# Kernel optimization log

Hardware: AMD Instinct MI355X
Metric: run time of the kernel (lower is better)

The kernel has to match this reference:

```python
import jax, jax.numpy as jnp
import numpy as np

DIM = 2048
DIM_HEAD = 64
HEADS = 16
FF_MULT = 4
LORA_R = 8
ATTN_INNER = DIM_HEAD * HEADS            # 1024
FF_INNER = DIM * FF_MULT                 # 8192
FUSED_DIMS = (ATTN_INNER, DIM_HEAD, DIM_HEAD, FF_INNER * 2)
B, N = 2, 2048


def setup_inputs() -> dict:
    key = jax.random.key(0)
    ks = jax.random.split(key, 12)
    s = 0.02
    inp = {
        "x": jax.random.normal(ks[0], (B, N, DIM), dtype=jnp.float32),
        "gamma": jnp.ones((DIM,), dtype=jnp.float32),
        "w_fused": jax.random.normal(ks[1], (DIM, sum(FUSED_DIMS)), dtype=jnp.float32) * s,
        "w_attn_out": jax.random.normal(ks[2], (ATTN_INNER, DIM), dtype=jnp.float32) * s,
        "w_ff_out": jax.random.normal(ks[3], (FF_INNER, DIM), dtype=jnp.float32) * s,
        "lora_q_a": jax.random.normal(ks[4], (DIM, LORA_R), dtype=jnp.float32) * s,
        "lora_q_b": jax.random.normal(ks[5], (LORA_R, ATTN_INNER), dtype=jnp.float32) * s,
        "lora_k_a": jax.random.normal(ks[6], (DIM, LORA_R), dtype=jnp.float32) * s,
        "lora_k_b": jax.random.normal(ks[7], (LORA_R, DIM_HEAD), dtype=jnp.float32) * s,
        "lora_v_a": jax.random.normal(ks[8], (DIM, LORA_R), dtype=jnp.float32) * s,
        "lora_v_b": jax.random.normal(ks[9], (LORA_R, DIM_HEAD), dtype=jnp.float32) * s,
        "lora_o_a": jax.random.normal(ks[10], (ATTN_INNER, LORA_R), dtype=jnp.float32) * s,
        "lora_o_b": jax.random.normal(ks[11], (LORA_R, DIM), dtype=jnp.float32) * s,
    }
    return inp


def _rotate_half(x):
    x1, x2 = jnp.split(x, 2, axis=-1)
    return jnp.concatenate((-x2, x1), axis=-1)


def _rope(pos, t):
    return t * jnp.cos(pos) + _rotate_half(t) * jnp.sin(pos)


def _forward(x, gamma, w_fused, w_attn_out, w_ff_out,
             lora_q_a, lora_q_b, lora_k_a, lora_k_b,
             lora_v_a, lora_v_b, lora_o_a, lora_o_b):
    b, n, d = x.shape
    # LayerNorm (beta = 0)
    mu = jnp.mean(x, axis=-1, keepdims=True)
    var = jnp.var(x, axis=-1, keepdims=True)
    xn = (x - mu) * jax.lax.rsqrt(var + 1e-5) * gamma

    fused = xn @ w_fused
    i0, i1, i2 = np.cumsum(FUSED_DIMS)[:3]
    q, k, v, ff = fused[..., :i0], fused[..., i0:i1], fused[..., i1:i2], fused[..., i2:]

    # LoRA additive terms
    q = q + (xn @ lora_q_a) @ lora_q_b
    k = k + (xn @ lora_k_a) @ lora_k_b
    v = v + (xn @ lora_v_a) @ lora_v_b

    q = q.reshape(b, n, HEADS, DIM_HEAD).transpose(0, 2, 1, 3)  # b h n d
    q = q * (DIM_HEAD ** -0.5)

    # rotary embedding: pos (n, dim_head)
    inv_freq = 1.0 / (10000.0 ** (jnp.arange(0, DIM_HEAD, 2, dtype=jnp.float32) / DIM_HEAD))
    freqs = jnp.arange(n, dtype=jnp.float32)[:, None] * inv_freq[None, :]
    pos = jnp.concatenate((freqs, freqs), axis=-1)
    q = _rope(pos, q)
    k = _rope(pos, k)  # k is b n d (multi-query, single kv head)

    sim = jnp.einsum('bhid,bjd->bhij', q, k)
    causal = jnp.triu(jnp.ones((n, n), dtype=bool), k=1)
    sim = jnp.where(causal, -jnp.finfo(sim.dtype).max, sim)
    attn = jax.nn.softmax(sim, axis=-1)
    out = jnp.einsum('bhij,bjd->bhid', attn, v)
    out = out.transpose(0, 2, 1, 3).reshape(b, n, ATTN_INNER)

    attn_out = out @ w_attn_out + (out @ lora_o_a) @ lora_o_b

    # SwiGLU: chunk -> (x_ff, gate); silu(gate) * x_ff
    x_ff, gate = jnp.split(ff, 2, axis=-1)
    ff_out = (jax.nn.silu(gate) * x_ff) @ w_ff_out

    return attn_out + ff_out


def reference(x, gamma, w_fused, w_attn_out, w_ff_out,
              lora_q_a, lora_q_b, lora_k_a, lora_k_b,
              lora_v_a, lora_v_b, lora_o_a, lora_o_b):
    return _forward(x, gamma, w_fused, w_attn_out, w_ff_out,
                    lora_q_a, lora_q_b, lora_k_a, lora_k_b,
                    lora_v_a, lora_v_b, lora_o_a, lora_o_b)
```

## Files before the change

kernel.cpp:

```cpp
#include <hip/hip_runtime.h>
#include <cstdint>


typedef __bf16 bf16_t;
typedef __bf16 bf16x8 __attribute__((ext_vector_type(8)));
typedef float f32x4 __attribute__((ext_vector_type(4)));

#define LOG2E 1.44269504088896340736f
#define LOG2_10K 13.287712379549449f

__device__ __forceinline__ void gload_lds16(const void* g, void* l) {
  __builtin_amdgcn_global_load_lds(
      (__attribute__((address_space(1))) void*)(uintptr_t)g,
      (__attribute__((address_space(3))) void*)(uint32_t)(uintptr_t)l,
      16, 0, 0);
}

__device__ __forceinline__ f32x4 mfma16(bf16x8 a, bf16x8 b, f32x4 c) {
  return __builtin_amdgcn_mfma_f32_16x16x32_bf16(a, b, c, 0, 0, 0);
}

__global__ __launch_bounds__(256) void ln_kernel(
    const float* __restrict__ x, const float* __restrict__ gamma,
    bf16_t* __restrict__ xn)
{
  const int row = blockIdx.x;
  const int t = threadIdx.x;
  const float4* xr = (const float4*)(x + (size_t)row * 2048);
  float4 a = xr[t * 2];
  float4 b = xr[t * 2 + 1];
  float s  = a.x + a.y + a.z + a.w + b.x + b.y + b.z + b.w;
  float ss = a.x*a.x + a.y*a.y + a.z*a.z + a.w*a.w
           + b.x*b.x + b.y*b.y + b.z*b.z + b.w*b.w;
  #pragma unroll
  for (int m = 1; m < 64; m <<= 1) {
    s  += __shfl_xor(s, m);
    ss += __shfl_xor(ss, m);
  }
  __shared__ float red[8];
  const int wave = t >> 6, lane = t & 63;
  if (lane == 0) { red[wave] = s; red[4 + wave] = ss; }
  __syncthreads();
  const float stot  = red[0] + red[1] + red[2] + red[3];
  const float sstot = red[4] + red[5] + red[6] + red[7];
  const float mu  = stot * (1.f / 2048.f);
  const float var = sstot * (1.f / 2048.f) - mu * mu;
  const float rs  = rsqrtf(var + 1e-5f);
  float v[8] = {a.x, a.y, a.z, a.w, b.x, b.y, b.z, b.w};
  bf16x8 o;
  #pragma unroll
  for (int e = 0; e < 8; ++e)
    o[e] = (bf16_t)((v[e] - mu) * rs * gamma[t * 8 + e]);
  *(bf16x8*)(xn + (size_t)row * 2048 + t * 8) = o;
}

__global__ __launch_bounds__(256) void transpose_wf_kernel(
    const float* __restrict__ w,
    const float* __restrict__ qa, const float* __restrict__ qb,
    const float* __restrict__ ka, const float* __restrict__ kb,
    const float* __restrict__ va, const float* __restrict__ vb,
    bf16_t* __restrict__ wfT)
{
  __shared__ float tile[64][65];
  const int t  = threadIdx.x;
  const int n0 = blockIdx.x * 64;
  const int k0 = blockIdx.y * 64;
  #pragma unroll
  for (int it = 0; it < 4; ++it) {
    const int kr = (t >> 4) + it * 16;
    const float4 vv = *(const float4*)(w + (size_t)(k0 + kr) * 17536 + n0 + (t & 15) * 4);
    tile[kr][(t & 15) * 4 + 0] = vv.x;
    tile[kr][(t & 15) * 4 + 1] = vv.y;
    tile[kr][(t & 15) * 4 + 2] = vv.z;
    tile[kr][(t & 15) * 4 + 3] = vv.w;
  }
  __syncthreads();
  const float* la = nullptr; const float* lb = nullptr;
  int nbo = 0, ldlb = 0;
  if (n0 < 1024)      { la = qa; lb = qb; nbo = n0;        ldlb = 1024; }
  else if (n0 < 1088) { la = ka; lb = kb; nbo = n0 - 1024; ldlb = 64;   }
  else if (n0 < 1152) { la = va; lb = vb; nbo = n0 - 1088; ldlb = 64;   }
  #pragma unroll
  for (int it = 0; it < 2; ++it) {
    const int nl = (t >> 3) + it * 32;
    const int kl = (t & 7) * 8;
    float vals[8];
    #pragma unroll
    for (int e = 0; e < 8; ++e) vals[e] = tile[kl + e][nl];
    if (la) {
      float bc[8];
      #pragma unroll
      for (int r = 0; r < 8; ++r) bc[r] = lb[r * ldlb + nbo + nl];
      #pragma unroll
      for (int e = 0; e < 8; ++e) {
        const float* ar = la + (size_t)(k0 + kl + e) * 8;
        float d = 0.f;
        #pragma unroll
        for (int r = 0; r < 8; ++r) d += ar[r] * bc[r];
        vals[e] += d;
      }
    }
    bf16x8 o;
    #pragma unroll
    for (int e = 0; e < 8; ++e) o[e] = (bf16_t)vals[e];
    *(bf16x8*)(wfT + (size_t)(n0 + nl) * 2048 + k0 + kl) = o;
  }
}

__global__ __launch_bounds__(256) void transpose_w2_kernel(
    const float* __restrict__ wff,
    const float* __restrict__ watt,
    const float* __restrict__ oa, const float* __restrict__ ob,
    bf16_t* __restrict__ w2T)
{
  __shared__ float tile[64][65];
  const int t  = threadIdx.x;
  const int n0 = blockIdx.x * 64;
  const int k0 = blockIdx.y * 64;
  const bool isatt = (k0 >= 8192);
  const float* src = isatt ? (watt + (size_t)(k0 - 8192) * 2048)
                           : (wff + (size_t)k0 * 2048);
  #pragma unroll
  for (int it = 0; it < 4; ++it) {
    const int kr = (t >> 4) + it * 16;
    const float4 vv = *(const float4*)(src + (size_t)kr * 2048 + n0 + (t & 15) * 4);
    tile[kr][(t & 15) * 4 + 0] = vv.x;
    tile[kr][(t & 15) * 4 + 1] = vv.y;
    tile[kr][(t & 15) * 4 + 2] = vv.z;
    tile[kr][(t & 15) * 4 + 3] = vv.w;
  }
  __syncthreads();
  #pragma unroll
  for (int it = 0; it < 2; ++it) {
    const int nl = (t >> 3) + it * 32;
    const int kl = (t & 7) * 8;
    float vals[8];
    #pragma unroll
    for (int e = 0; e < 8; ++e) vals[e] = tile[kl + e][nl];
    if (isatt) {
      float bc[8];
      #pragma unroll
      for (int r = 0; r < 8; ++r) bc[r] = ob[r * 2048 + n0 + nl];
      #pragma unroll
      for (int e = 0; e < 8; ++e) {
        const float* ar = oa + (size_t)(k0 - 8192 + kl + e) * 8;
        float d = 0.f;
        #pragma unroll
        for (int r = 0; r < 8; ++r) d += ar[r] * bc[r];
        vals[e] += d;
      }
    }
    bf16x8 o;
    #pragma unroll
    for (int e = 0; e < 8; ++e) o[e] = (bf16_t)vals[e];
    *(bf16x8*)(w2T + (size_t)(n0 + nl) * 9216 + k0 + kl) = o;
  }
}

__device__ __forceinline__ void gemm_core_128x128(
    const bf16_t* __restrict__ A, int ldA, int m0,
    const bf16_t* __restrict__ BT, int ldB, int n0,
    int K, bf16_t* As, bf16_t* Bs, f32x4* acc)
{
  const int t = threadIdx.x;
  const int wave = t >> 6;
  const int lane = t & 63;
  const int quad = lane >> 4;
  const int ln15 = lane & 15;
  const int wm = wave & 1, wn = wave >> 1;

  const bf16_t* gA = A + (size_t)(m0 + (t >> 2)) * ldA + ((t & 3) << 3);
  const bf16_t* gB = BT + (size_t)(n0 + (t >> 2)) * ldB + ((t & 3) << 3);
  char* lA = (char*)As + wave * 1024;
  char* lB = (char*)Bs + wave * 1024;
  const size_t sA64 = (size_t)64 * ldA;
  const size_t sB64 = (size_t)64 * ldB;
  const int aoff = (wm * 64 + ln15) * 32 + quad * 8;
  const int boff = (wn * 64 + ln15) * 32 + quad * 8;

  for (int kt = 0; kt < K; kt += 32) {
    gload_lds16(gA,        lA);
    gload_lds16(gA + sA64, lA + 4096);
    gload_lds16(gB,        lB);
    gload_lds16(gB + sB64, lB + 4096);
    gA += 32;
    gB += 32;
    __syncthreads();
    bf16x8 a0 = *(const bf16x8*)(As + aoff);
    bf16x8 a1 = *(const bf16x8*)(As + aoff + 512);
    bf16x8 a2 = *(const bf16x8*)(As + aoff + 1024);
    bf16x8 a3 = *(const bf16x8*)(As + aoff + 1536);
    bf16x8 b0 = *(const bf16x8*)(Bs + boff);
    bf16x8 b1 = *(const bf16x8*)(Bs + boff + 512);
    bf16x8 b2 = *(const bf16x8*)(Bs + boff + 1024);
    bf16x8 b3 = *(const bf16x8*)(Bs + boff + 1536);
    acc[0]  = mfma16(a0, b0, acc[0]);
    acc[1]  = mfma16(a0, b1, acc[1]);
    acc[2]  = mfma16(a0, b2, acc[2]);
    acc[3]  = mfma16(a0, b3, acc[3]);
    acc[4]  = mfma16(a1, b0, acc[4]);
    acc[5]  = mfma16(a1, b1, acc[5]);
    acc[6]  = mfma16(a1, b2, acc[6]);
    acc[7]  = mfma16(a1, b3, acc[7]);
    acc[8]  = mfma16(a2, b0, acc[8]);
    acc[9]  = mfma16(a2, b1, acc[9]);
    acc[10] = mfma16(a2, b2, acc[10]);
    acc[11] = mfma16(a2, b3, acc[11]);
    acc[12] = mfma16(a3, b0, acc[12]);
    acc[13] = mfma16(a3, b1, acc[13]);
    acc[14] = mfma16(a3, b2, acc[14]);
    acc[15] = mfma16(a3, b3, acc[15]);
    __syncthreads();
  }
}

__device__ __forceinline__ void gemm_core_dual(
    const bf16_t* gA, const bf16_t* gB0, const bf16_t* gB1,
    int ldA, int ldB, int K,
    bf16_t* As, bf16_t* B0s, bf16_t* B1s,
    f32x4* acc0, f32x4* acc1)
{
  const int t = threadIdx.x;
  const int wave = t >> 6;
  const int lane = t & 63;
  const int quad = lane >> 4;
  const int ln15 = lane & 15;
  const int wm = wave & 1, wn = wave >> 1;

  char* lA = (char*)As + wave * 1024;
  char* l0 = (char*)B0s + wave * 1024;
  char* l1 = (char*)B1s + wave * 1024;
  const size_t sA64 = (size_t)64 * ldA;
  const size_t sB64 = (size_t)64 * ldB;
  const int aoff = (wm * 64 + ln15) * 32 + quad * 8;
  const int boff = (wn * 64 + ln15) * 32 + quad * 8;

  for (int kt = 0; kt < K; kt += 32) {
    gload_lds16(gA,         lA);
    gload_lds16(gA + sA64,  lA + 4096);
    gload_lds16(gB0,        l0);
    gload_lds16(gB0 + sB64, l0 + 4096);
    gload_lds16(gB1,        l1);
    gload_lds16(gB1 + sB64, l1 + 4096);
    gA += 32; gB0 += 32; gB1 += 32;
    __syncthreads();
    bf16x8 a0 = *(const bf16x8*)(As + aoff);
    bf16x8 a1 = *(const bf16x8*)(As + aoff + 512);
    bf16x8 a2 = *(const bf16x8*)(As + aoff + 1024);
    bf16x8 a3 = *(const bf16x8*)(As + aoff + 1536);
    bf16x8 p0 = *(const bf16x8*)(B0s + boff);
    bf16x8 p1 = *(const bf16x8*)(B0s + boff + 512);
    bf16x8 p2 = *(const bf16x8*)(B0s + boff + 1024);
    bf16x8 p3 = *(const bf16x8*)(B0s + boff + 1536);
    bf16x8 q0 = *(const bf16x8*)(B1s + boff);
    bf16x8 q1 = *(const bf16x8*)(B1s + boff + 512);
    bf16x8 q2 = *(const bf16x8*)(B1s + boff + 1024);
    bf16x8 q3 = *(const bf16x8*)(B1s + boff + 1536);
    acc0[0]  = mfma16(a0, p0, acc0[0]);
    acc0[1]  = mfma16(a0, p1, acc0[1]);
    acc0[2]  = mfma16(a0, p2, acc0[2]);
    acc0[3]  = mfma16(a0, p3, acc0[3]);
    acc1[0]  = mfma16(a0, q0, acc1[0]);
    acc1[1]  = mfma16(a0, q1, acc1[1]);
    acc1[2]  = mfma16(a0, q2, acc1[2]);
    acc1[3]  = mfma16(a0, q3, acc1[3]);
    acc0[4]  = mfma16(a1, p0, acc0[4]);
    acc0[5]  = mfma16(a1, p1, acc0[5]);
    acc0[6]  = mfma16(a1, p2, acc0[6]);
    acc0[7]  = mfma16(a1, p3, acc0[7]);
    acc1[4]  = mfma16(a1, q0, acc1[4]);
    acc1[5]  = mfma16(a1, q1, acc1[5]);
    acc1[6]  = mfma16(a1, q2, acc1[6]);
    acc1[7]  = mfma16(a1, q3, acc1[7]);
    acc0[8]  = mfma16(a2, p0, acc0[8]);
    acc0[9]  = mfma16(a2, p1, acc0[9]);
    acc0[10] = mfma16(a2, p2, acc0[10]);
    acc0[11] = mfma16(a2, p3, acc0[11]);
    acc1[8]  = mfma16(a2, q0, acc1[8]);
    acc1[9]  = mfma16(a2, q1, acc1[9]);
    acc1[10] = mfma16(a2, q2, acc1[10]);
    acc1[11] = mfma16(a2, q3, acc1[11]);
    acc0[12] = mfma16(a3, p0, acc0[12]);
    acc0[13] = mfma16(a3, p1, acc0[13]);
    acc0[14] = mfma16(a3, p2, acc0[14]);
    acc0[15] = mfma16(a3, p3, acc0[15]);
    acc1[12] = mfma16(a3, q0, acc1[12]);
    acc1[13] = mfma16(a3, q1, acc1[13]);
    acc1[14] = mfma16(a3, q2, acc1[14]);
    acc1[15] = mfma16(a3, q3, acc1[15]);
    __syncthreads();
  }
}

__global__ __launch_bounds__(256, 2) void gemm1_qkv_kernel(
    const bf16_t* __restrict__ xn, const bf16_t* __restrict__ wfT,
    bf16_t* __restrict__ Q, bf16_t* __restrict__ K, bf16_t* __restrict__ Vt)
{
  __shared__ __align__(16) bf16_t As[128 * 32];
  __shared__ __align__(16) bf16_t B0s[128 * 32];
  __shared__ __align__(16) bf16_t B1s[128 * 32];
  const int m0 = blockIdx.x * 128;
  const int y = blockIdx.y;
  const int t = threadIdx.x;
  const int wave = t >> 6, lane = t & 63;
  const int quad = lane >> 4, ln15 = lane & 15;
  const int wm = wave & 1, wn = wave >> 1;

  const int rb = m0 + wm * 64 + quad * 4;
  const float invf0 = exp2f(-(float)ln15 * (LOG2_10K / 32.0f));
  const float invf1 = exp2f(-(float)(16 + ln15) * (LOG2_10K / 32.0f));

  if (y < 4) {
    const bf16_t* gA  = xn  + (size_t)(m0 + (t >> 2)) * 2048 + ((t & 3) << 3);
    const bf16_t* gB0 = wfT + (size_t)(y * 256 + (t >> 2)) * 2048 + ((t & 3) << 3);
    const bf16_t* gB1 = wfT + (size_t)(y * 256 + 128 + (t >> 2)) * 2048 + ((t & 3) << 3);
    f32x4 acc0[16], acc1[16];
    #pragma unroll
    for (int f = 0; f < 16; ++f) {
      acc0[f] = (f32x4){0.f, 0.f, 0.f, 0.f};
      acc1[f] = (f32x4){0.f, 0.f, 0.f, 0.f};
    }
    gemm_core_dual(gA, gB0, gB1, 2048, 2048, 2048, As, B0s, B1s, acc0, acc1);
    #pragma unroll
    for (int half = 0; half < 2; ++half) {
      const f32x4* acc = half ? acc1 : acc0;
      const int hd = y * 4 + half * 2 + wn;
      #pragma unroll
      for (int i = 0; i < 4; ++i) {
        #pragma unroll
        for (int rr = 0; rr < 4; ++rr) {
          const int row = rb + i * 16 + rr;
          const int b = row >> 11, n = row & 2047;
          const float fn = (float)n;
          float s0, c0, s1, c1;
          __sincosf(fn * invf0, &s0, &c0);
          __sincosf(fn * invf1, &s1, &c1);
          float vals[4];
          #pragma unroll
          for (int j = 0; j < 4; ++j) vals[j] = acc[i * 4 + j][rr];
          #pragma unroll
          for (int j = 0; j < 4; ++j) {
            const float rot = (j < 2) ? -vals[j + 2] : vals[j - 2];
            const float c = (j & 1) ? c1 : c0;
            const float s = (j & 1) ? s1 : s0;
            const float o = (vals[j] * c + rot * s) * 0.125f;
            Q[(((size_t)b * 16 + hd) * 2048 + n) * 64 + j * 16 + ln15] = (bf16_t)o;
          }
        }
      }
    }
  } else {
    f32x4 acc[16];
    #pragma unroll
    for (int f = 0; f < 16; ++f) acc[f] = (f32x4){0.f, 0.f, 0.f, 0.f};
    gemm_core_128x128(xn, 2048, m0, wfT, 2048, 1024, 2048, As, B0s, acc);
    const bool is_k = (wn == 0);
    #pragma unroll
    for (int i = 0; i < 4; ++i) {
      #pragma unroll
      for (int rr = 0; rr < 4; ++rr) {
        const int row = rb + i * 16 + rr;
        const int b = row >> 11, n = row & 2047;
        float vals[4];
        #pragma unroll
        for (int j = 0; j < 4; ++j) vals[j] = acc[i * 4 + j][rr];
        if (is_k) {
          const float fn = (float)n;
          float s0, c0, s1, c1;
          __sincosf(fn * invf0, &s0, &c0);
          __sincosf(fn * invf1, &s1, &c1);
          #pragma unroll
          for (int j = 0; j < 4; ++j) {
            const float rot = (j < 2) ? -vals[j + 2] : vals[j - 2];
            const float c = (j & 1) ? c1 : c0;
            const float s = (j & 1) ? s1 : s0;
            K[((size_t)b * 2048 + n) * 64 + j * 16 + ln15] = (bf16_t)(vals[j] * c + rot * s);
          }
        } else {
          #pragma unroll
          for (int j = 0; j < 4; ++j)
            Vt[((size_t)b * 64 + j * 16 + ln15) * 2048 + n] = (bf16_t)vals[j];
        }
      }
    }
  }
}


#define FF_STG() {                                                           \
    char* lA_ = lds + sst + w * 1024;                                        \
    gload_lds16(gA, lA_);                                                    \
    gload_lds16(gA + (size_t)128 * 2048, lA_ + 8192);                        \
    char* lB_ = lds + 65536 + sst + w * 1024;                                \
    gload_lds16(gB0, lB_);                                                   \
    gload_lds16(gB1, lB_ + 8192);                                            \
    gA += 32; gB0 += 32; gB1 += 32;                                          \
    sst = (sst + 16384) & 65535; }

#define FF_RD(DA, DB) {                                                      \
    _Pragma("unroll")                                                        \
    for (int mf_ = 0; mf_ < 8; ++mf_)                                        \
      DA[mf_] = *(const bf16x8*)(lds + srd + wm * 8192 + mf_ * 1024 + ro);   \
    _Pragma("unroll")                                                        \
    for (int nf_ = 0; nf_ < 4; ++nf_)                                        \
      DB[nf_] = *(const bf16x8*)(lds + 65536 + srd + wn * 4096 + nf_ * 1024 + ro); \
    srd = (srd + 16384) & 65535; }

#define FF_MM(SA, SB) {                                                      \
    __builtin_amdgcn_s_setprio(1);                                           \
    _Pragma("unroll")                                                        \
    for (int mf_ = 0; mf_ < 8; ++mf_) {                                      \
      _Pragma("unroll")                                                      \
      for (int nf_ = 0; nf_ < 4; ++nf_)                                      \
        acc[mf_][nf_] = mfma16(SA[mf_], SB[nf_], acc[mf_][nf_]);             \
    }                                                                        \
    __builtin_amdgcn_s_setprio(0); }

#define FF_SYNC4() { asm volatile("s_waitcnt vmcnt(4)" ::: "memory");        \
    __builtin_amdgcn_s_barrier(); }

__global__ __launch_bounds__(512, 2) void gemm1_ff_kernel(
    const bf16_t* __restrict__ xn, const bf16_t* __restrict__ wfT,
    bf16_t* __restrict__ A2)
{
  __shared__ __align__(16) char lds[131072];
  const int m0 = blockIdx.x * 256;
  const int c0 = blockIdx.y * 128;
  const int t = threadIdx.x;
  const int w = t >> 6, lane = t & 63;
  const int quad = lane >> 4, ln15 = lane & 15;
  const int wm = w & 1, wn = w >> 1;

  const int p  = w * 64 + lane;
  const int r  = p >> 2;
  const int cl = (p & 3) ^ ((r >> 1) & 3);
  const bf16_t* gA = xn + (size_t)(m0 + r) * 2048 + cl * 8;
  const int r2 = r + 128;
  const int cm0 = c0 + ((r  >> 5) << 4) + (r  & 15);
  const int cm1 = c0 + ((r2 >> 5) << 4) + (r2 & 15);
  const int wr0 = ((r  >> 4) & 1) ? (1152 + cm0) : (9344 + cm0);
  const int wr1 = ((r2 >> 4) & 1) ? (1152 + cm1) : (9344 + cm1);
  const bf16_t* gB0 = wfT + (size_t)wr0 * 2048 + cl * 8;
  const bf16_t* gB1 = wfT + (size_t)wr1 * 2048 + cl * 8;

  const int ro = ln15 * 64 + ((quad ^ ((ln15 >> 1) & 3)) * 16);

  f32x4 acc[8][4];
  #pragma unroll
  for (int mf = 0; mf < 8; ++mf)
    #pragma unroll
    for (int nf = 0; nf < 4; ++nf)
      acc[mf][nf] = (f32x4){0.f, 0.f, 0.f, 0.f};

  int sst = 0, srd = 0;
  #pragma unroll
  for (int pt = 0; pt < 3; ++pt) FF_STG();
  FF_SYNC4();

  bf16x8 fA[8], fB[4], nA[8], nB[4];
  FF_RD(fA, fB);

  for (int i = 0; i < 30; ++i) {
    FF_STG(); FF_RD(nA, nB); FF_MM(fA, fB); FF_SYNC4();
    FF_STG(); FF_RD(fA, fB); FF_MM(nA, nB); FF_SYNC4();
  }
  FF_STG(); FF_RD(nA, nB); FF_MM(fA, fB); FF_SYNC4();
  FF_RD(fA, fB); FF_MM(nA, nB);
  asm volatile("s_waitcnt vmcnt(0)" ::: "memory");
  __builtin_amdgcn_s_barrier();
  FF_RD(nA, nB); FF_MM(fA, fB);
  FF_MM(nA, nB);

  const int row0 = m0 + wm * 128 + quad * 4;
  const int col0 = c0 + wn * 32 + ln15;
  #pragma unroll
  for (int mf = 0; mf < 8; ++mf)
    #pragma unroll
    for (int rr = 0; rr < 4; ++rr) {
      bf16_t* dst = A2 + (size_t)(row0 + mf * 16 + rr) * 9216 + col0;
      #pragma unroll
      for (int j = 0; j < 2; ++j) {
        const float g  = acc[mf][2 * j][rr];
        const float xv = acc[mf][2 * j + 1][rr];
        dst[j * 16] = (bf16_t)(xv * (g / (1.f + exp2f(-g * LOG2E))));
      }
    }
}

#define G2_STG() {                                                           \
    char* lA_ = lds + sstA + w * 1024;                                       \
    gload_lds16(gA, lA_);                                                    \
    gload_lds16(gA + (size_t)128 * 9216, lA_ + 8192);                        \
    gload_lds16(gB, lds + 65536 + sstB + w * 1024);                          \
    gA += 32; gB += 32;                                                      \
    sstA = (sstA + 16384) & 65535;                                           \
    sstB = (sstB + 8192) & 32767; }

#define G2_RD(DA, DB) {                                                      \
    _Pragma("unroll")                                                        \
    for (int mf_ = 0; mf_ < 4; ++mf_)                                        \
      DA[mf_] = *(const bf16x8*)(lds + srdA + wm * 4096 + mf_ * 1024 + ro);  \
    _Pragma("unroll")                                                        \
    for (int nf_ = 0; nf_ < 4; ++nf_)                                        \
      DB[nf_] = *(const bf16x8*)(lds + 65536 + srdB + wn * 4096 + nf_ * 1024 + ro); \
    srdA = (srdA + 16384) & 65535;                                           \
    srdB = (srdB + 8192) & 32767; }

#define G2_MM(SA, SB) {                                                      \
    __builtin_amdgcn_s_setprio(1);                                           \
    _Pragma("unroll")                                                        \
    for (int mf_ = 0; mf_ < 4; ++mf_) {                                      \
      _Pragma("unroll")                                                      \
      for (int nf_ = 0; nf_ < 4; ++nf_)                                      \
        acc[mf_][nf_] = mfma16(SA[mf_], SB[nf_], acc[mf_][nf_]);             \
    }                                                                        \
    __builtin_amdgcn_s_setprio(0); }

#define G2_SYNC3() { asm volatile("s_waitcnt vmcnt(3)" ::: "memory");        \
    __builtin_amdgcn_s_barrier(); }

__global__ __launch_bounds__(512, 2) void gemm2_kernel(
    const bf16_t* __restrict__ A2, const bf16_t* __restrict__ w2T,
    float* __restrict__ out)
{
  __shared__ __align__(16) char lds[98304];
  const int m0 = blockIdx.x * 256;
  const int n0 = blockIdx.y * 128;
  const int t = threadIdx.x;
  const int w = t >> 6, lane = t & 63;
  const int quad = lane >> 4, ln15 = lane & 15;
  const int wm = w & 3, wn = w >> 2;

  const int p  = w * 64 + lane;
  const int r  = p >> 2;
  const int cl = (p & 3) ^ ((r >> 1) & 3);
  const bf16_t* gA = A2  + (size_t)(m0 + r) * 9216 + cl * 8;
  const bf16_t* gB = w2T + (size_t)(n0 + r) * 9216 + cl * 8;

  const int ro = ln15 * 64 + ((quad ^ ((ln15 >> 1) & 3)) * 16);

  f32x4 acc[4][4];
  #pragma unroll
  for (int mf = 0; mf < 4; ++mf)
    #pragma unroll
    for (int nf = 0; nf < 4; ++nf)
      acc[mf][nf] = (f32x4){0.f, 0.f, 0.f, 0.f};

  int sstA = 0, sstB = 0, srdA = 0, srdB = 0;
  #pragma unroll
  for (int pt = 0; pt < 3; ++pt) G2_STG();
  G2_SYNC3();

  bf16x8 fA[4], fB[4], nA[4], nB[4];
  G2_RD(fA, fB);

  for (int i = 0; i < 142; ++i) {
    G2_STG(); G2_RD(nA, nB); G2_MM(fA, fB); G2_SYNC3();
    G2_STG(); G2_RD(fA, fB); G2_MM(nA, nB); G2_SYNC3();
  }
  G2_STG(); G2_RD(nA, nB); G2_MM(fA, fB); G2_SYNC3();
  G2_RD(fA, fB); G2_MM(nA, nB);
  asm volatile("s_waitcnt vmcnt(0)" ::: "memory");
  __builtin_amdgcn_s_barrier();
  G2_RD(nA, nB); G2_MM(fA, fB);
  G2_MM(nA, nB);

  const int row0 = m0 + wm * 64 + quad * 4;
  const int col0 = n0 + wn * 64 + ln15;
  #pragma unroll
  for (int mf = 0; mf < 4; ++mf)
    #pragma unroll
    for (int rr = 0; rr < 4; ++rr) {
      float* dst = out + (size_t)(row0 + mf * 16 + rr) * 2048 + col0;
      #pragma unroll
      for (int nf = 0; nf < 4; ++nf)
        dst[nf * 16] = acc[mf][nf][rr];
    }
}

__global__ __launch_bounds__(256, 2) void attn_kernel(
    const bf16_t* __restrict__ Q, const bf16_t* __restrict__ Kg_,
    const bf16_t* __restrict__ Vt, bf16_t* __restrict__ A2)
{
  __shared__ __align__(16) bf16_t Qs[64 * 64];
  __shared__ __align__(16) bf16_t Ks[64 * 64];
  __shared__ __align__(16) bf16_t Vs[64 * 64];
  __shared__ __align__(16) bf16_t Ps[64 * 64];
  const int pidx = blockIdx.x, bh = blockIdx.y;
  const int b = bh >> 4, h = bh & 15;
  const int t = threadIdx.x;
  const int wave = t >> 6, lane = t & 63;
  const int quad = lane >> 4, ln15 = lane & 15;

  const bf16_t* Kg = Kg_ + (size_t)b * 2048 * 64;
  const bf16_t* Vg = Vt + (size_t)b * 64 * 2048;

  for (int hlf = 0; hlf < 2; ++hlf) {
    const int qt = hlf ? (31 - pidx) : pidx;
    const int qm0 = qt * 64;
    const bf16_t* Qg = Q + ((size_t)bh * 2048 + qm0) * 64;

    {
      const bf16_t* g = Qg + (size_t)(t >> 3) * 64 + ((t & 7) << 3);
      char* l = (char*)Qs + wave * 1024;
      gload_lds16(g,           l);
      gload_lds16(g + 32 * 64, l + 4096);
    }

    float mstate[4], lstate[4];
    f32x4 o_acc[4];
    #pragma unroll
    for (int rr = 0; rr < 4; ++rr) { mstate[rr] = -1e30f; lstate[rr] = 0.f; }
    #pragma unroll
    for (int jd = 0; jd < 4; ++jd) o_acc[jd] = (f32x4){0.f, 0.f, 0.f, 0.f};

    const int njt = qt + 1;
    for (int jt = 0; jt < njt; ++jt) {
      {
        const bf16_t* kg = Kg + (size_t)(jt * 64 + (t >> 3)) * 64 + ((t & 7) << 3);
        char* lk = (char*)Ks + wave * 1024;
        gload_lds16(kg,           lk);
        gload_lds16(kg + 32 * 64, lk + 4096);
        const bf16_t* vg = Vg + (size_t)(t >> 3) * 2048 + jt * 64 + ((t & 7) << 3);
        char* lv = (char*)Vs + wave * 1024;
        gload_lds16(vg,                   lv);
        gload_lds16(vg + (size_t)32*2048, lv + 4096);
      }
      __syncthreads();

      f32x4 sA[4];
      #pragma unroll
      for (int j = 0; j < 4; ++j) sA[j] = (f32x4){0.f, 0.f, 0.f, 0.f};
      #pragma unroll
      for (int ks = 0; ks < 2; ++ks) {
        bf16x8 aq = *(const bf16x8*)(Qs + (wave * 16 + ln15) * 64 + ks * 32 + quad * 8);
        #pragma unroll
        for (int j = 0; j < 4; ++j) {
          bf16x8 bk = *(const bf16x8*)(Ks + (j * 16 + ln15) * 64 + ks * 32 + quad * 8);
          sA[j] = mfma16(aq, bk, sA[j]);
        }
      }

      const bool needmask = (jt * 64 + 63 > qm0 + wave * 16);
      const int row0 = qm0 + wave * 16 + quad * 4;
      float alpha[4];
      #pragma unroll
      for (int rr = 0; rr < 4; ++rr) {
        const int rowg = row0 + rr;
        if (needmask) {
          #pragma unroll
          for (int j = 0; j < 4; ++j) {
            const int colg = jt * 64 + j * 16 + ln15;
            if (colg > rowg) sA[j][rr] = -1e30f;
          }
        }
        float mx = fmaxf(fmaxf(sA[0][rr], sA[1][rr]),
                         fmaxf(sA[2][rr], sA[3][rr]));
        mx = fmaxf(mx, __shfl_xor(mx, 1));
        mx = fmaxf(mx, __shfl_xor(mx, 2));
        mx = fmaxf(mx, __shfl_xor(mx, 4));
        mx = fmaxf(mx, __shfl_xor(mx, 8));
        const float mold = mstate[rr];
        const float mnew = fmaxf(mold, mx);
        const float al = exp2f((mold - mnew) * LOG2E);
        float rsum = 0.f;
        #pragma unroll
        for (int j = 0; j < 4; ++j) {
          const float p = exp2f((sA[j][rr] - mnew) * LOG2E);
          sA[j][rr] = p;
          rsum += p;
        }
        rsum += __shfl_xor(rsum, 1);
        rsum += __shfl_xor(rsum, 2);
        rsum += __shfl_xor(rsum, 4);
        rsum += __shfl_xor(rsum, 8);
        lstate[rr] = lstate[rr] * al + rsum;
        mstate[rr] = mnew;
        alpha[rr] = al;
      }
      #pragma unroll
      for (int jd = 0; jd < 4; ++jd)
        #pragma unroll
        for (int rr = 0; rr < 4; ++rr)
          o_acc[jd][rr] *= alpha[rr];
      #pragma unroll
      for (int j = 0; j < 4; ++j)
        #pragma unroll
        for (int rr = 0; rr < 4; ++rr)
          Ps[wave * 1024 + (quad * 4 + rr) * 64 + j * 16 + ln15] = (bf16_t)sA[j][rr];

      #pragma unroll
      for (int ks = 0; ks < 2; ++ks) {
        bf16x8 ap = *(const bf16x8*)(Ps + wave * 1024 + ln15 * 64 + ks * 32 + quad * 8);
        #pragma unroll
        for (int jd = 0; jd < 4; ++jd) {
          bf16x8 bv = *(const bf16x8*)(Vs + (jd * 16 + ln15) * 64 + ks * 32 + quad * 8);
          o_acc[jd] = mfma16(ap, bv, o_acc[jd]);
        }
      }
      __syncthreads();
    }

    const int row0 = qm0 + wave * 16 + quad * 4;
    #pragma unroll
    for (int rr = 0; rr < 4; ++rr) {
      const float inv = 1.f / lstate[rr];
      bf16_t* dst = A2 + ((size_t)b * 2048 + row0 + rr) * 9216 + 8192 + h * 64 + ln15;
      #pragma unroll
      for (int jd = 0; jd < 4; ++jd)
        dst[jd * 16] = (bf16_t)(o_acc[jd][rr] * inv);
    }
  }
}

extern "C" void kernel_launch(void* const* d_in, const int* in_sizes, int n_in,
                              void* d_out, int out_size, void* d_ws, size_t ws_size,
                              hipStream_t stream)
{
  const float* x      = (const float*)d_in[0];
  const float* gamma  = (const float*)d_in[1];
  const float* wfused = (const float*)d_in[2];
  const float* watt   = (const float*)d_in[3];
  const float* wff    = (const float*)d_in[4];
  const float* qa     = (const float*)d_in[5];
  const float* qb     = (const float*)d_in[6];
  const float* ka     = (const float*)d_in[7];
  const float* kb     = (const float*)d_in[8];
  const float* va     = (const float*)d_in[9];
  const float* vb     = (const float*)d_in[10];
  const float* oa     = (const float*)d_in[11];
  const float* ob     = (const float*)d_in[12];
  float* out = (float*)d_out;

  char* ws = (char*)d_ws;
  bf16_t* xn  = (bf16_t*)(ws);
  bf16_t* wfT = (bf16_t*)(ws + 16777216);
  bf16_t* w2T = (bf16_t*)(ws + 88604672);
  bf16_t* A2  = (bf16_t*)(ws + 126353408);
  bf16_t* Qr  = (bf16_t*)(ws + 201850880);
  bf16_t* Kr  = (bf16_t*)(ws + 210239488);
  bf16_t* Vtr = (bf16_t*)(ws + 210763776);

  ln_kernel<<<dim3(4096), dim3(256), 0, stream>>>(x, gamma, xn);
  transpose_wf_kernel<<<dim3(274, 32), dim3(256), 0, stream>>>(
      wfused, qa, qb, ka, kb, va, vb, wfT);
  transpose_w2_kernel<<<dim3(32, 144), dim3(256), 0, stream>>>(
      wff, watt, oa, ob, w2T);
  gemm1_qkv_kernel<<<dim3(32, 5), dim3(256), 0, stream>>>(xn, wfT, Qr, Kr, Vtr);
  gemm1_ff_kernel<<<dim3(16, 64), dim3(512), 0, stream>>>(xn, wfT, A2);
  attn_kernel<<<dim3(16, 32), dim3(256), 0, stream>>>(Qr, Kr, Vtr, A2);
  gemm2_kernel<<<dim3(16, 16), dim3(512), 0, stream>>>(A2, w2T, out);
}
```

Baseline: 876.9 us.

## Restructure GEMM pipelines into triple-buffered split phases and smaller gemm2 tiles

The FF GEMM main loop is reorganized into two half-phases per K-step: one stages A and computes the first half of the M fragments, the other stages B and computes the second half. Barriers sit between the LDS reads and the MFMAs, and a sched_barrier fences them, so fragment registers drop to one set and LDS drops to three buffers. gemm2 moves to 128x128 tiles with 256 threads and 4 blocks per CU, using the same triple-buffered single-phase pipeline. The aim is better overlap of global-to-LDS loads with MFMA and higher occupancy, at the cost of more barriers per K-step and more A/B reloads for the smaller gemm2 tiles.

After: 897.1 us. +2.3%, slower.

```diff
diff --git a/kernel.cpp b/kernel.cpp
--- a/kernel.cpp
+++ b/kernel.cpp
@@ -8,6 +8,9 @@
 
 #define LOG2E 1.44269504088896340736f
 #define LOG2_10K 13.287712379549449f
+
+#define WAITCNT_VM(N) __builtin_amdgcn_s_waitcnt(0x0F70 | (N))
+#define WAITCNT_LGKM() __builtin_amdgcn_s_waitcnt(0xC07F)
 
 __device__ __forceinline__ void gload_lds16(const void* g, void* l) {
   __builtin_amdgcn_global_load_lds(
@@ -387,43 +390,59 @@
 }
 
 
-#define FF_STG() {                                                           \
-    char* lA_ = lds + sst + w * 1024;                                        \
-    gload_lds16(gA, lA_);                                                    \
-    gload_lds16(gA + (size_t)128 * 2048, lA_ + 8192);                        \
-    char* lB_ = lds + 65536 + sst + w * 1024;                                \
-    gload_lds16(gB0, lB_);                                                   \
-    gload_lds16(gB1, lB_ + 8192);                                            \
-    gA += 32; gB0 += 32; gB1 += 32;                                          \
-    sst = (sst + 16384) & 65535; }
-
-#define FF_RD(DA, DB) {                                                      \
-    _Pragma("unroll")                                                        \
-    for (int mf_ = 0; mf_ < 8; ++mf_)                                        \
-      DA[mf_] = *(const bf16x8*)(lds + srd + wm * 8192 + mf_ * 1024 + ro);   \
+#define FF_PHA(STG) {                                                        \
+    if (STG) {                                                               \
+      char* d_ = lds + nb + w * 1024;                                        \
+      gload_lds16(gA, d_);                                                   \
+      gload_lds16(gA + (size_t)128 * 2048, d_ + 8192);                       \
+    }                                                                        \
     _Pragma("unroll")                                                        \
     for (int nf_ = 0; nf_ < 4; ++nf_)                                        \
-      DB[nf_] = *(const bf16x8*)(lds + 65536 + srd + wn * 4096 + nf_ * 1024 + ro); \
-    srd = (srd + 16384) & 65535; }
-
-#define FF_MM(SA, SB) {                                                      \
+      fB[nf_] = *(const bf16x8*)(lds + cb + 16384 + wn * 4096 + nf_ * 1024 + ro); \
+    _Pragma("unroll")                                                        \
+    for (int mf_ = 0; mf_ < 4; ++mf_)                                        \
+      fA[mf_] = *(const bf16x8*)(lds + cb + wm * 8192 + mf_ * 1024 + ro);    \
+    __builtin_amdgcn_s_barrier();                                            \
+    WAITCNT_LGKM();                                                          \
+    __builtin_amdgcn_sched_barrier(0);                                       \
     __builtin_amdgcn_s_setprio(1);                                           \
     _Pragma("unroll")                                                        \
-    for (int mf_ = 0; mf_ < 8; ++mf_) {                                      \
+    for (int mf_ = 0; mf_ < 4; ++mf_) {                                      \
       _Pragma("unroll")                                                      \
       for (int nf_ = 0; nf_ < 4; ++nf_)                                      \
-        acc[mf_][nf_] = mfma16(SA[mf_], SB[nf_], acc[mf_][nf_]);             \
+        acc[mf_][nf_] = mfma16(fA[mf_], fB[nf_], acc[mf_][nf_]);             \
     }                                                                        \
-    __builtin_amdgcn_s_setprio(0); }
-
-#define FF_SYNC4() { asm volatile("s_waitcnt vmcnt(4)" ::: "memory");        \
+    __builtin_amdgcn_s_setprio(0);                                           \
+    __builtin_amdgcn_s_barrier(); }
+
+#define FF_PHB(STG, VMW) {                                                   \
+    if (STG) {                                                               \
+      char* d_ = lds + nb + 16384 + w * 1024;                                \
+      gload_lds16(gB0, d_);                                                  \
+      gload_lds16(gB1, d_ + 8192);                                           \
+    }                                                                        \
+    _Pragma("unroll")                                                        \
+    for (int mf_ = 0; mf_ < 4; ++mf_)                                        \
+      fA[mf_] = *(const bf16x8*)(lds + cb + wm * 8192 + (4 + mf_) * 1024 + ro); \
+    __builtin_amdgcn_s_barrier();                                            \
+    WAITCNT_LGKM();                                                          \
+    __builtin_amdgcn_sched_barrier(0);                                       \
+    __builtin_amdgcn_s_setprio(1);                                           \
+    _Pragma("unroll")                                                        \
+    for (int mf_ = 0; mf_ < 4; ++mf_) {                                      \
+      _Pragma("unroll")                                                      \
+      for (int nf_ = 0; nf_ < 4; ++nf_)                                      \
+        acc[4 + mf_][nf_] = mfma16(fA[mf_], fB[nf_], acc[4 + mf_][nf_]);     \
+    }                                                                        \
+    __builtin_amdgcn_s_setprio(0);                                           \
+    VMW;                                                                     \
     __builtin_amdgcn_s_barrier(); }
 
 __global__ __launch_bounds__(512, 2) void gemm1_ff_kernel(
     const bf16_t* __restrict__ xn, const bf16_t* __restrict__ wfT,
     bf16_t* __restrict__ A2)
 {
-  __shared__ __align__(16) char lds[131072];
+  __shared__ __align__(16) char lds[98304];
   const int m0 = blockIdx.x * 256;
   const int c0 = blockIdx.y * 128;
   const int t = threadIdx.x;
@@ -452,24 +471,40 @@
     for (int nf = 0; nf < 4; ++nf)
       acc[mf][nf] = (f32x4){0.f, 0.f, 0.f, 0.f};
 
-  int sst = 0, srd = 0;
-  #pragma unroll
-  for (int pt = 0; pt < 3; ++pt) FF_STG();
-  FF_SYNC4();
-
-  bf16x8 fA[8], fB[4], nA[8], nB[4];
-  FF_RD(fA, fB);
-
-  for (int i = 0; i < 30; ++i) {
-    FF_STG(); FF_RD(nA, nB); FF_MM(fA, fB); FF_SYNC4();
-    FF_STG(); FF_RD(fA, fB); FF_MM(nA, nB); FF_SYNC4();
-  }
-  FF_STG(); FF_RD(nA, nB); FF_MM(fA, fB); FF_SYNC4();
-  FF_RD(fA, fB); FF_MM(nA, nB);
-  asm volatile("s_waitcnt vmcnt(0)" ::: "memory");
+  {
+    char* d0 = lds + w * 1024;
+    gload_lds16(gA, d0);
+    gload_lds16(gA + (size_t)128 * 2048, d0 + 8192);
+    char* e0 = lds + 16384 + w * 1024;
+    gload_lds16(gB0, e0);
+    gload_lds16(gB1, e0 + 8192);
+    gA += 32; gB0 += 32; gB1 += 32;
+    char* d1 = lds + 32768 + w * 1024;
+    gload_lds16(gA, d1);
+    gload_lds16(gA + (size_t)128 * 2048, d1 + 8192);
+    char* e1 = lds + 32768 + 16384 + w * 1024;
+    gload_lds16(gB0, e1);
+    gload_lds16(gB1, e1 + 8192);
+    gA += 32; gB0 += 32; gB1 += 32;
+  }
+  WAITCNT_VM(4);
   __builtin_amdgcn_s_barrier();
-  FF_RD(nA, nB); FF_MM(fA, fB);
-  FF_MM(nA, nB);
+
+  int cb = 0, nb = 65536;
+  bf16x8 fA[4], fB[4];
+
+  for (int s = 0; s < 62; ++s) {
+    FF_PHA(true);
+    FF_PHB(true, WAITCNT_VM(4));
+    gA += 32; gB0 += 32; gB1 += 32;
+    cb = (cb == 65536) ? 0 : cb + 32768;
+    nb = (nb == 65536) ? 0 : nb + 32768;
+  }
+  FF_PHA(false);
+  FF_PHB(false, WAITCNT_VM(0));
+  cb = (cb == 65536) ? 0 : cb + 32768;
+  FF_PHA(false);
+  FF_PHB(false, ;);
 
   const int row0 = m0 + wm * 128 + quad * 4;
   const int col0 = c0 + wn * 32 + ln15;
@@ -487,51 +522,48 @@
     }
 }
 
-#define G2_STG() {                                                           \
-    char* lA_ = lds + sstA + w * 1024;                                       \
-    gload_lds16(gA, lA_);                                                    \
-    gload_lds16(gA + (size_t)128 * 9216, lA_ + 8192);                        \
-    gload_lds16(gB, lds + 65536 + sstB + w * 1024);                          \
-    gA += 32; gB += 32;                                                      \
-    sstA = (sstA + 16384) & 65535;                                           \
-    sstB = (sstB + 8192) & 32767; }
-
-#define G2_RD(DA, DB) {                                                      \
+#define G2_PH(STG, VMW) {                                                    \
+    if (STG) {                                                               \
+      char* dA_ = lds + nb + w * 1024;                                       \
+      gload_lds16(gA, dA_);                                                  \
+      gload_lds16(gA + (size_t)64 * 9216, dA_ + 4096);                       \
+      char* dB_ = lds + nb + 8192 + w * 1024;                                \
+      gload_lds16(gB, dB_);                                                  \
+      gload_lds16(gB + (size_t)64 * 9216, dB_ + 4096);                       \
+    }                                                                        \
+    _Pragma("unroll")                                                        \
+    for (int nf_ = 0; nf_ < 4; ++nf_)                                        \
+      fB[nf_] = *(const bf16x8*)(lds + cb + 8192 + wn * 4096 + nf_ * 1024 + ro); \
     _Pragma("unroll")                                                        \
     for (int mf_ = 0; mf_ < 4; ++mf_)                                        \
-      DA[mf_] = *(const bf16x8*)(lds + srdA + wm * 4096 + mf_ * 1024 + ro);  \
-    _Pragma("unroll")                                                        \
-    for (int nf_ = 0; nf_ < 4; ++nf_)                                        \
-      DB[nf_] = *(const bf16x8*)(lds + 65536 + srdB + wn * 4096 + nf_ * 1024 + ro); \
-    srdA = (srdA + 16384) & 65535;                                           \
-    srdB = (srdB + 8192) & 32767; }
-
-#define G2_MM(SA, SB) {                                                      \
+      fA[mf_] = *(const bf16x8*)(lds + cb + wm * 4096 + mf_ * 1024 + ro);    \
+    __builtin_amdgcn_s_barrier();                                            \
+    WAITCNT_LGKM();                                                          \
+    __builtin_amdgcn_sched_barrier(0);                                       \
     __builtin_amdgcn_s_setprio(1);                                           \
     _Pragma("unroll")                                                        \
     for (int mf_ = 0; mf_ < 4; ++mf_) {                                      \
       _Pragma("unroll")                                                      \
       for (int nf_ = 0; nf_ < 4; ++nf_)                                      \
-        acc[mf_][nf_] = mfma16(SA[mf_], SB[nf_], acc[mf_][nf_]);             \
+        acc[mf_][nf_] = mfma16(fA[mf_], fB[nf_], acc[mf_][nf_]);             \
     }                                                                        \
-    __builtin_amdgcn_s_setprio(0); }
-
-#define G2_SYNC3() { asm volatile("s_waitcnt vmcnt(3)" ::: "memory");        \
+    __builtin_amdgcn_s_setprio(0);                                           \
+    VMW;                                                                     \
     __builtin_amdgcn_s_barrier(); }
 
-__global__ __launch_bounds__(512, 2) void gemm2_kernel(
+__global__ __launch_bounds__(256, 4) void gemm2_kernel(
     const bf16_t* __restrict__ A2, const bf16_t* __restrict__ w2T,
     float* __restrict__ out)
 {
-  __shared__ __align__(16) char lds[98304];
-  const int m0 = blockIdx.x * 256;
+  __shared__ __align__(16) char lds[49152];
+  const int m0 = blockIdx.x * 128;
   const int n0 = blockIdx.y * 128;
   const int t = threadIdx.x;
   const int w = t >> 6, lane = t & 63;
   const int quad = lane >> 4, ln15 = lane & 15;
-  const int wm = w & 3, wn = w >> 2;
-
-  const int p  = w * 64 + lane;
+  const int wm = w & 1, wn = w >> 1;
+
+  const int p  = t;
   const int r  = p >> 2;
   const int cl = (p & 3) ^ ((r >> 1) & 3);
   const bf16_t* gA = A2  + (size_t)(m0 + r) * 9216 + cl * 8;
@@ -546,24 +578,37 @@
     for (int nf = 0; nf < 4; ++nf)
       acc[mf][nf] = (f32x4){0.f, 0.f, 0.f, 0.f};
 
-  int sstA = 0, sstB = 0, srdA = 0, srdB = 0;
-  #pragma unroll
-  for (int pt = 0; pt < 3; ++pt) G2_STG();
-  G2_SYNC3();
-
-  bf16x8 fA[4], fB[4], nA[4], nB[4];
-  G2_RD(fA, fB);
-
-  for (int i = 0; i < 142; ++i) {
-    G2_STG(); G2_RD(nA, nB); G2_MM(fA, fB); G2_SYNC3();
-    G2_STG(); G2_RD(fA, fB); G2_MM(nA, nB); G2_SYNC3();
-  }
-  G2_STG(); G2_RD(nA, nB); G2_MM(fA, fB); G2_SYNC3();
-  G2_RD(fA, fB); G2_MM(nA, nB);
-  asm volatile("s_waitcnt vmcnt(0)" ::: "memory");
+  {
+    char* dA0 = lds + w * 1024;
+    gload_lds16(gA, dA0);
+    gload_lds16(gA + (size_t)64 * 9216, dA0 + 4096);
+    char* dB0 = lds + 8192 + w * 1024;
+    gload_lds16(gB, dB0);
+    gload_lds16(gB + (size_t)64 * 9216, dB0 + 4096);
+    gA += 32; gB += 32;
+    char* dA1 = lds + 16384 + w * 1024;
+    gload_lds16(gA, dA1);
+    gload_lds16(gA + (size_t)64 * 9216, dA1 + 4096);
+    char* dB1 = lds + 16384 + 8192 + w * 1024;
+    gload_lds16(gB, dB1);
+    gload_lds16(gB + (size_t)64 * 9216, dB1 + 4096);
+    gA += 32; gB += 32;
+  }
+  WAITCNT_VM(4);
   __builtin_amdgcn_s_barrier();
-  G2_RD(nA, nB); G2_MM(fA, fB);
-  G2_MM(nA, nB);
+
+  int cb = 0, nb = 32768;
+  bf16x8 fA[4], fB[4];
+
+  for (int s = 0; s < 286; ++s) {
+    G2_PH(true, WAITCNT_VM(4));
+    gA += 32; gB += 32;
+    cb = (cb == 32768) ? 0 : cb + 16384;
+    nb = (nb == 32768) ? 0 : nb + 16384;
+  }
+  G2_PH(false, WAITCNT_VM(0));
+  cb = (cb == 32768) ? 0 : cb + 16384;
+  G2_PH(false, ;);
 
   const int row0 = m0 + wm * 64 + quad * 4;
   const int col0 = n0 + wn * 64 + ln15;
@@ -749,5 +794,5 @@
   gemm1_qkv_kernel<<<dim3(32, 5), dim3(256), 0, stream>>>(xn, wfT, Qr, Kr, Vtr);
   gemm1_ff_kernel<<<dim3(16, 64), dim3(512), 0, stream>>>(xn, wfT, A2);
   attn_kernel<<<dim3(16, 32), dim3(256), 0, stream>>>(Qr, Kr, Vtr, A2);
-  gemm2_kernel<<<dim3(16, 16), dim3(512), 0, stream>>>(A2, w2T, out);
-}
+  gemm2_kernel<<<dim3(32, 16), dim3(256), 0, stream>>>(A2, w2T, out);
+}
```
